# Kernel optimization log

Measured on AMD Instinct MI355X. Metric: run time of the kernel, lower is better.

The kernel has to match this reference:

```python
import jax, jax.numpy as jnp
import numpy as np

DIM, HIDDEN, E = 1024, 4096, 8
B, L = 2, 2048


def setup_inputs() -> dict:
    key = jax.random.key(0)
    ks = jax.random.split(key, 6)
    s_in = 1.0 / np.sqrt(DIM)
    s_h = 1.0 / np.sqrt(HIDDEN)
    return {
        "x": jax.random.normal(ks[0], (B, L, DIM), dtype=jnp.float32),
        "Wg": jax.random.uniform(ks[1], (E, DIM), jnp.float32, -s_in, s_in),
        "W1": jax.random.uniform(ks[2], (E, DIM, HIDDEN), jnp.float32, -s_in, s_in),
        "b1": jax.random.uniform(ks[3], (E, HIDDEN), jnp.float32, -s_in, s_in),
        "W2": jax.random.uniform(ks[4], (E, HIDDEN, DIM), jnp.float32, -s_h, s_h),
        "b2": jax.random.uniform(ks[5], (E, DIM), jnp.float32, -s_h, s_h),
    }


def reference(x, Wg, W1, b1, W2, b2):
    # Router: top-1 over gate logits (softmax is monotone, argmax of probs == argmax of logits)
    gate_logits = jnp.einsum("bld,ed->ble", x, Wg)  # [B, L, E]
    top1 = jnp.argmax(gate_logits, axis=-1)          # [B, L] int
    out = jnp.zeros_like(x)
    # Fixed small loop over experts (structurally distinct weights); per-expert
    # dense MLP + select, honoring top-1 dispatch/combine semantics.
    for e in range(E):
        mask = (top1 == e)[..., None]                                   # [B, L, 1]
        h = jax.nn.gelu(jnp.einsum("bld,dh->blh", x, W1[e]) + b1[e],
                        approximate=False)                              # [B, L, H]
        y = jnp.einsum("blh,hd->bld", h, W2[e]) + b2[e]                 # [B, L, D]
        out = jnp.where(mask, y, out)
    return out
```

## Files before the change

kernel.cpp:

```cpp
#include <hip/hip_runtime.h>
#include <hip/hip_bf16.h>
#include <math.h>

#define NTOK 4096
#define DIMSZ 1024
#define HID 4096
#define NE 8
#define RT_MAX 40

typedef unsigned short u16;
typedef unsigned int u32;
typedef __attribute__((ext_vector_type(8))) short bf16x8;
typedef __attribute__((ext_vector_type(4))) float f32x4;

static __device__ __forceinline__ u16 f2bf(float f) {
    u32 u = __float_as_uint(f);
    u32 r = u + 0x7fffu + ((u >> 16) & 1u);
    return (u16)(r >> 16);
}

static __device__ __forceinline__ u32 pk2bf(float lo, float hi) {
    __hip_bfloat162 h = __float22bfloat162_rn(make_float2(lo, hi));
    return *(u32*)&h;
}

__global__ void k_init(int* counts, int* cursor) {
    if (threadIdx.x < NE) { counts[threadIdx.x] = 0; cursor[threadIdx.x] = 0; }
}

__global__ __launch_bounds__(256) void k_router(const float* __restrict__ x,
                                                const float* __restrict__ Wg,
                                                int* __restrict__ ids,
                                                int* __restrict__ counts) {
    int wave = threadIdx.x >> 6;
    int lane = threadIdx.x & 63;
    int t = blockIdx.x * 4 + wave;

    const float4* xr = (const float4*)(x + (size_t)t * DIMSZ);
    float4 xv[4];
#pragma unroll
    for (int j = 0; j < 4; j++) xv[j] = xr[j * 64 + lane];

    float s[NE];
#pragma unroll
    for (int e = 0; e < NE; e++) {
        const float4* wr = (const float4*)(Wg + (size_t)e * DIMSZ);
        float p = 0.f;
#pragma unroll
        for (int j = 0; j < 4; j++) {
            float4 w = wr[j * 64 + lane];
            p += xv[j].x * w.x + xv[j].y * w.y + xv[j].z * w.z + xv[j].w * w.w;
        }
#pragma unroll
        for (int m = 32; m >= 1; m >>= 1) p += __shfl_xor(p, m, 64);
        s[e] = p;
    }
    if (lane == 0) {
        int best = 0;
#pragma unroll
        for (int e = 1; e < NE; e++) if (s[e] > s[best]) best = e;
        ids[t] = best;
        atomicAdd(&counts[best], 1);
    }
}

__global__ void k_scan(const int* __restrict__ counts, int* __restrict__ offs) {
    if (threadIdx.x == 0) {
        int a = 0;
        for (int e = 0; e < NE; e++) { offs[e] = a; a += counts[e]; }
    }
}

__global__ __launch_bounds__(256) void k_gather(const float* __restrict__ x,
                                                const int* __restrict__ ids,
                                                const int* __restrict__ offs,
                                                int* __restrict__ cursor,
                                                int* __restrict__ perm,
                                                u16* __restrict__ Xg) {
    int t = blockIdx.x;
    __shared__ int sp;
    if (threadIdx.x == 0) {
        int e = ids[t];
        int p = offs[e] + atomicAdd(&cursor[e], 1);
        perm[p] = t;
        sp = p;
    }
    __syncthreads();
    int p = sp;
    const float4* src = (const float4*)(x + (size_t)t * DIMSZ);
    float4 v = src[threadIdx.x];
    u32 w0 = pk2bf(v.x, v.y);
    u32 w1 = pk2bf(v.z, v.w);
    uint2* dst = (uint2*)(Xg + (size_t)p * DIMSZ + threadIdx.x * 4);
    *dst = make_uint2(w0, w1);
}

template <int KDIM, int NDIM, int EPI>
__global__ __launch_bounds__(256) void k_gemm(const u16* __restrict__ A,
                                              const float* __restrict__ Ball,
                                              const float* __restrict__ biasAll,
                                              const int* __restrict__ counts,
                                              const int* __restrict__ offs,
                                              const int* __restrict__ perm,
                                              u16* __restrict__ Hout,
                                              float* __restrict__ Fout) {
    constexpr int NT = NDIM / 128;
    constexpr int NWG = RT_MAX * NT;
    constexpr int CPX = NWG / 8;
    constexpr int NK = KDIM / 64;
    int bid = blockIdx.x;
    int wid = (bid & 7) * CPX + (bid >> 3);
    int x = wid % RT_MAX;
    int n0 = (wid / RT_MAX) * 128;

    int e = -1, lrt = 0, a0 = 0;
#pragma unroll
    for (int i = 0; i < NE; i++) {
        int rt = (counts[i] + 127) >> 7;
        if (e < 0 && x < a0 + rt) { e = i; lrt = x - a0; }
        a0 += rt;
    }
    if (e < 0) return;
    int row0 = offs[e] + lrt * 128;
    int nrows = offs[e] + counts[e] - row0;
    if (nrows > 128) nrows = 128;

    __shared__ alignas(16) u16 As[2][128][64];
    __shared__ alignas(16) u16 Bs[2][128][64];

    int tid = threadIdx.x;
    int lane = tid & 63;
    int wave = tid >> 6;
    int wr = wave >> 1, wc = wave & 1;

    const u16* srcA[4];
#pragma unroll
    for (int p = 0; p < 4; p++) {
        int g = p * 256 + tid;
        int r = g >> 3, slot = g & 7;
        int rc = r < nrows ? r : nrows - 1;
        srcA[p] = A + (size_t)(row0 + rc) * KDIM + ((slot ^ (r & 7)) * 8);
    }
    int bn4 = (tid & 31) * 4;
    int bkb = tid >> 5;
    const float* srcB = Ball + (size_t)e * KDIM * NDIM + (size_t)(bkb * 8) * NDIM + n0 + bn4;

    f32x4 acc[4][4] = {};
    int fr = lane & 15, fc = lane >> 4;

    float4 breg[8];

#define LOAD_B(KK)                                                              \
    {                                                                           \
        const float* bp = srcB + (size_t)(KK) * 64 * NDIM;                      \
        _Pragma("unroll")                                                       \
        for (int j = 0; j < 8; j++) breg[j] = *(const float4*)(bp + (size_t)j * NDIM); \
    }

#define STAGE_A(BUF, KK)                                                        \
    {                                                                           \
        _Pragma("unroll")                                                       \
        for (int p = 0; p < 4; p++) {                                           \
            __builtin_amdgcn_global_load_lds(                                   \
                (const __attribute__((address_space(1))) void*)(srcA[p] + (KK) * 64), \
                (__attribute__((address_space(3))) void*)((u16*)&As[BUF][0][0] + (p * 256 + wave * 64) * 8), \
                16, 0, 0);                                                      \
        }                                                                       \
    }

#define WRITE_B(BUF)                                                            \
    {                                                                           \
        const float* vf = (const float*)breg;                                   \
        _Pragma("unroll")                                                       \
        for (int i = 0; i < 4; i++) {                                           \
            int N = bn4 + i;                                                    \
            u32 w0 = pk2bf(vf[0 + i],  vf[4 + i]);                              \
            u32 w1 = pk2bf(vf[8 + i],  vf[12 + i]);                             \
            u32 w2 = pk2bf(vf[16 + i], vf[20 + i]);                             \
            u32 w3 = pk2bf(vf[24 + i], vf[28 + i]);                             \
            u32 off = (u32)(bkb * 16) ^ (u32)((N & 7) << 4);                    \
            *(uint4*)((char*)&Bs[BUF][N][0] + off) = make_uint4(w0, w1, w2, w3); \
        }                                                                       \
    }

    LOAD_B(0);
    STAGE_A(0, 0);
    WRITE_B(0);
    __syncthreads();

    for (int kk = 0; kk < NK; kk++) {
        int cur = kk & 1;
        if (kk + 1 < NK) {
            LOAD_B(kk + 1);
            STAGE_A(cur ^ 1, kk + 1);
        }
#pragma unroll
        for (int k2 = 0; k2 < 2; k2++) {
            bf16x8 af[4], bfr[4];
#pragma unroll
            for (int m = 0; m < 4; m++) {
                int r = wr * 64 + m * 16 + fr;
                u32 off = (u32)(k2 * 64 + fc * 16) ^ (u32)((r & 7) << 4);
                af[m] = *(const bf16x8*)((const char*)&As[cur][r][0] + off);
            }
#pragma unroll
            for (int n = 0; n < 4; n++) {
                int N = wc * 64 + n * 16 + fr;
                u32 off = (u32)(k2 * 64 + fc * 16) ^ (u32)((N & 7) << 4);
                bfr[n] = *(const bf16x8*)((const char*)&Bs[cur][N][0] + off);
            }
#pragma unroll
            for (int m = 0; m < 4; m++)
#pragma unroll
                for (int n = 0; n < 4; n++)
                    acc[m][n] = __builtin_amdgcn_mfma_f32_16x16x32_bf16(af[m], bfr[n], acc[m][n], 0, 0, 0);
        }
        if (kk + 1 < NK) {
            WRITE_B(cur ^ 1);
            __syncthreads();
        }
    }
#undef LOAD_B
#undef STAGE_A
#undef WRITE_B

    int cb = lane & 15;
    int rq = lane >> 4;
#pragma unroll
    for (int m = 0; m < 4; m++) {
        int rbase = wr * 64 + m * 16 + rq * 4;
#pragma unroll
        for (int n = 0; n < 4; n++) {
            int col = n0 + wc * 64 + n * 16 + cb;
            float bias = biasAll[(size_t)e * NDIM + col];
#pragma unroll
            for (int j = 0; j < 4; j++) {
                int r = rbase + j;
                if (r < nrows) {
                    float v = acc[m][n][j] + bias;
                    int p = row0 + r;
                    if (EPI == 1) {
                        float g = 0.5f * v * (1.0f + erff(v * 0.70710678118654752f));
                        Hout[(size_t)p * NDIM + col] = f2bf(g);
                    } else {
                        int trow = perm[p];
                        Fout[(size_t)trow * NDIM + col] = v;
                    }
                }
            }
        }
    }
}

extern "C" void kernel_launch(void* const* d_in, const int* in_sizes, int n_in,
                              void* d_out, int out_size, void* d_ws, size_t ws_size,
                              hipStream_t stream) {
    const float* x  = (const float*)d_in[0];
    const float* Wg = (const float*)d_in[1];
    const float* W1 = (const float*)d_in[2];
    const float* b1 = (const float*)d_in[3];
    const float* W2 = (const float*)d_in[4];
    const float* b2 = (const float*)d_in[5];
    float* out = (float*)d_out;

    char* ws = (char*)d_ws;
    int* ids    = (int*)(ws + 0);
    int* counts = (int*)(ws + 16384);
    int* offs   = (int*)(ws + 16448);
    int* cursor = (int*)(ws + 16512);
    int* perm   = (int*)(ws + 16576);
    u16* Xg     = (u16*)(ws + 33024);
    u16* H      = (u16*)(ws + 33024 + 8388608);

    k_init<<<dim3(1), dim3(64), 0, stream>>>(counts, cursor);
    k_router<<<dim3(NTOK / 4), dim3(256), 0, stream>>>(x, Wg, ids, counts);
    k_scan<<<dim3(1), dim3(64), 0, stream>>>(counts, offs);
    k_gather<<<dim3(NTOK), dim3(256), 0, stream>>>(x, ids, offs, cursor, perm, Xg);
    k_gemm<DIMSZ, HID, 1><<<dim3(RT_MAX * (HID / 128)), dim3(256), 0, stream>>>(
        Xg, W1, b1, counts, offs, perm, H, (float*)nullptr);
    k_gemm<HID, DIMSZ, 2><<<dim3(RT_MAX * (DIMSZ / 128)), dim3(256), 0, stream>>>(
        H, W2, b2, counts, offs, perm, (u16*)nullptr, out);
}
```

Baseline: 380.3 us.

## Triple-buffer A tiles with explicit vmcnt waits to deepen GEMM pipeline

Restructures the grouped expert GEMM main loop so A tiles (loaded directly into LDS) use three rotating buffers and B loads run one more stage ahead. Explicit s_waitcnt vmcnt counts and raw s_barrier replace __syncthreads, so global loads for tile k+2 can stay in flight while tile k is computed. The aim is to hide global memory latency better. In exchange it uses more LDS, which can reduce occupancy, and it depends on hand-computed vmcnt counts being correct.

```diff
diff --git a/kernel.cpp b/kernel.cpp
--- a/kernel.cpp
+++ b/kernel.cpp
@@ -125,8 +125,8 @@
     int nrows = offs[e] + counts[e] - row0;
     if (nrows > 128) nrows = 128;
 
-    __shared__ alignas(16) u16 As[2][128][64];
-    __shared__ alignas(16) u16 Bs[2][128][64];
+    __shared__ alignas(16) u16 Asb[3][128][64];
+    __shared__ alignas(16) u16 Bsb[2][128][64];
 
     int tid = threadIdx.x;
     int lane = tid & 63;
@@ -149,26 +149,28 @@
     int fr = lane & 15, fc = lane >> 4;
 
     float4 breg[8];
-
-#define LOAD_B(KK)                                                              \
+    u16 *Ar = &Asb[0][0][0], *An = &Asb[1][0][0], *Aw = &Asb[2][0][0];
+    u16 *Br = &Bsb[0][0][0], *Bw = &Bsb[1][0][0];
+
+#define LOAD_B(KT)                                                              \
     {                                                                           \
-        const float* bp = srcB + (size_t)(KK) * 64 * NDIM;                      \
+        const float* bp = srcB + (size_t)(KT) * 64 * NDIM;                      \
         _Pragma("unroll")                                                       \
         for (int j = 0; j < 8; j++) breg[j] = *(const float4*)(bp + (size_t)j * NDIM); \
     }
 
-#define STAGE_A(BUF, KK)                                                        \
+#define STAGE_A(DST, KT)                                                        \
     {                                                                           \
         _Pragma("unroll")                                                       \
         for (int p = 0; p < 4; p++) {                                           \
             __builtin_amdgcn_global_load_lds(                                   \
-                (const __attribute__((address_space(1))) void*)(srcA[p] + (KK) * 64), \
-                (__attribute__((address_space(3))) void*)((u16*)&As[BUF][0][0] + (p * 256 + wave * 64) * 8), \
+                (const __attribute__((address_space(1))) void*)(srcA[p] + (KT) * 64), \
+                (__attribute__((address_space(3))) void*)((DST) + (p * 256 + wave * 64) * 8), \
                 16, 0, 0);                                                      \
         }                                                                       \
     }
 
-#define WRITE_B(BUF)                                                            \
+#define WRITE_B(DST)                                                            \
     {                                                                           \
         const float* vf = (const float*)breg;                                   \
         _Pragma("unroll")                                                       \
@@ -179,50 +181,77 @@
             u32 w2 = pk2bf(vf[16 + i], vf[20 + i]);                             \
             u32 w3 = pk2bf(vf[24 + i], vf[28 + i]);                             \
             u32 off = (u32)(bkb * 16) ^ (u32)((N & 7) << 4);                    \
-            *(uint4*)((char*)&Bs[BUF][N][0] + off) = make_uint4(w0, w1, w2, w3); \
+            *(uint4*)((char*)(DST) + N * 128 + off) = make_uint4(w0, w1, w2, w3); \
         }                                                                       \
     }
 
+#define COMPUTE()                                                               \
+    {                                                                           \
+        _Pragma("unroll")                                                       \
+        for (int k2 = 0; k2 < 2; k2++) {                                        \
+            bf16x8 af[4], bfr[4];                                               \
+            _Pragma("unroll")                                                   \
+            for (int m = 0; m < 4; m++) {                                       \
+                int r = wr * 64 + m * 16 + fr;                                  \
+                u32 off = (u32)(k2 * 64 + fc * 16) ^ (u32)((r & 7) << 4);       \
+                af[m] = *(const bf16x8*)((const char*)Ar + r * 128 + off);      \
+            }                                                                   \
+            _Pragma("unroll")                                                   \
+            for (int n = 0; n < 4; n++) {                                       \
+                int N = wc * 64 + n * 16 + fr;                                  \
+                u32 off = (u32)(k2 * 64 + fc * 16) ^ (u32)((N & 7) << 4);       \
+                bfr[n] = *(const bf16x8*)((const char*)Br + N * 128 + off);     \
+            }                                                                   \
+            _Pragma("unroll")                                                   \
+            for (int m = 0; m < 4; m++)                                         \
+                _Pragma("unroll")                                               \
+                for (int n = 0; n < 4; n++)                                     \
+                    acc[m][n] = __builtin_amdgcn_mfma_f32_16x16x32_bf16(af[m], bfr[n], acc[m][n], 0, 0, 0); \
+        }                                                                       \
+    }
+
+#define WAITV(N) asm volatile("s_waitcnt vmcnt(" #N ")" ::: "memory")
+#define WAITL()  asm volatile("s_waitcnt lgkmcnt(0)" ::: "memory")
+#define BAR()    __builtin_amdgcn_s_barrier()
+
     LOAD_B(0);
-    STAGE_A(0, 0);
-    WRITE_B(0);
-    __syncthreads();
-
-    for (int kk = 0; kk < NK; kk++) {
-        int cur = kk & 1;
-        if (kk + 1 < NK) {
-            LOAD_B(kk + 1);
-            STAGE_A(cur ^ 1, kk + 1);
-        }
-#pragma unroll
-        for (int k2 = 0; k2 < 2; k2++) {
-            bf16x8 af[4], bfr[4];
-#pragma unroll
-            for (int m = 0; m < 4; m++) {
-                int r = wr * 64 + m * 16 + fr;
-                u32 off = (u32)(k2 * 64 + fc * 16) ^ (u32)((r & 7) << 4);
-                af[m] = *(const bf16x8*)((const char*)&As[cur][r][0] + off);
-            }
-#pragma unroll
-            for (int n = 0; n < 4; n++) {
-                int N = wc * 64 + n * 16 + fr;
-                u32 off = (u32)(k2 * 64 + fc * 16) ^ (u32)((N & 7) << 4);
-                bfr[n] = *(const bf16x8*)((const char*)&Bs[cur][N][0] + off);
-            }
-#pragma unroll
-            for (int m = 0; m < 4; m++)
-#pragma unroll
-                for (int n = 0; n < 4; n++)
-                    acc[m][n] = __builtin_amdgcn_mfma_f32_16x16x32_bf16(af[m], bfr[n], acc[m][n], 0, 0, 0);
-        }
-        if (kk + 1 < NK) {
-            WRITE_B(cur ^ 1);
-            __syncthreads();
-        }
-    }
+    STAGE_A(Ar, 0);
+    WAITV(4);
+    WRITE_B(Br);
+    LOAD_B(1);
+    STAGE_A(An, 1);
+    WAITV(12);
+    WAITL();
+    BAR();
+
+    for (int kk = 0; kk < NK - 2; kk++) {
+        COMPUTE();
+        WAITV(4);
+        WRITE_B(Bw);
+        LOAD_B(kk + 2);
+        STAGE_A(Aw, kk + 2);
+        WAITV(12);
+        WAITL();
+        BAR();
+        u16* t = Ar; Ar = An; An = Aw; Aw = t;
+        t = Br; Br = Bw; Bw = t;
+    }
+    COMPUTE();
+    WAITV(4);
+    WRITE_B(Bw);
+    WAITV(0);
+    WAITL();
+    BAR();
+    { u16* t = Ar; Ar = An; An = Aw; Aw = t; t = Br; Br = Bw; Bw = t; }
+    COMPUTE();
+
 #undef LOAD_B
 #undef STAGE_A
 #undef WRITE_B
+#undef COMPUTE
+#undef WAITV
+#undef WAITL
+#undef BAR
 
     int cb = lane & 15;
     int rq = lane >> 4;
```

New measurement: 311.4 us (median of 3 runs). 18.1% less time.
